# Optimization experiments

Hardware: AMD Instinct MI355X
Metric: run time of the kernel (lower is better)

## Reference

```python
import jax, jax.numpy as jnp
import numpy as np

N_HEAD, D_MODEL, D_K, D_V = 16, 1024, 64, 64
LN_EPS = 1e-5


def setup_inputs() -> dict:
    key = jax.random.key(0)
    ks = jax.random.split(key, 10)
    B, S = 2, 2048
    s = 1.0 / np.sqrt(D_MODEL)
    return {
        "q": jax.random.normal(ks[0], (B, S, D_MODEL), jnp.float32),
        "k": jax.random.normal(ks[1], (B, S, D_MODEL), jnp.float32),
        "v": jax.random.normal(ks[2], (B, S, D_MODEL), jnp.float32),
        "w_q": jax.random.normal(ks[3], (D_MODEL, N_HEAD * D_K), jnp.float32) * s,
        "w_k": jax.random.normal(ks[4], (D_MODEL, N_HEAD * D_K), jnp.float32) * s,
        "w_v": jax.random.normal(ks[5], (D_MODEL, N_HEAD * D_V), jnp.float32) * s,
        "w_fc": jax.random.normal(ks[6], (N_HEAD * D_V, D_MODEL), jnp.float32) * s,
        "b_fc": jnp.zeros((D_MODEL,), jnp.float32),
        "ln_g": jnp.ones((D_MODEL,), jnp.float32),
        "ln_b": jnp.zeros((D_MODEL,), jnp.float32),
    }


def _mha(q, k, v, w_q, w_k, w_v, w_fc, b_fc, ln_g, ln_b):
    B, S, _ = q.shape
    residual = q
    # projections -> [B, H, S, Dh]
    qh = (q @ w_q).reshape(B, S, N_HEAD, D_K).transpose(0, 2, 1, 3)
    kh = (k @ w_k).reshape(B, S, N_HEAD, D_K).transpose(0, 2, 1, 3)
    vh = (v @ w_v).reshape(B, S, N_HEAD, D_V).transpose(0, 2, 1, 3)
    # NOTE: original scales by sqrt(d_model), not sqrt(d_k)
    temper = jnp.sqrt(jnp.asarray(D_MODEL, qh.dtype))
    attn = jnp.einsum("bhqd,bhkd->bhqk", qh, kh) / temper
    attn = jax.nn.softmax(attn, axis=-1)  # dropout = identity (eval mode)
    out = jnp.einsum("bhqk,bhkd->bhqd", attn, vh)
    out = out.transpose(0, 2, 1, 3).reshape(B, S, N_HEAD * D_V)
    out = out @ w_fc + b_fc  # dropout = identity (eval mode)
    x = out + residual
    mu = jnp.mean(x, axis=-1, keepdims=True)
    var = jnp.var(x, axis=-1, keepdims=True)
    x = (x - mu) * jax.lax.rsqrt(var + LN_EPS) * ln_g + ln_b
    return x, attn


def reference(q, k, v, w_q, w_k, w_v, w_fc, b_fc, ln_g, ln_b):
    return _mha(q, k, v, w_q, w_k, w_v, w_fc, b_fc, ln_g, ln_b)
```

## Files before the change

### kernel.cpp

```cpp
#include <hip/hip_runtime.h>
#include <hip/hip_bf16.h>
#include <stdint.h>

typedef __attribute__((ext_vector_type(8))) short bf16x8;
typedef __attribute__((ext_vector_type(4))) float f32x4;

#define GLOAD16(gptr, lptr)                                              \
  __builtin_amdgcn_global_load_lds(                                      \
      (const __attribute__((address_space(1))) void*)(gptr),             \
      (__attribute__((address_space(3))) void*)(lptr), 16, 0, 0)

__device__ __forceinline__ uint32_t pack_bf16_2(float a, float b) {
  union { __hip_bfloat16 h; unsigned short u; } ca, cb;
  ca.h = __float2bfloat16(a); cb.h = __float2bfloat16(b);
  return (uint32_t)ca.u | ((uint32_t)cb.u << 16);
}

__global__ __launch_bounds__(256)
void cvt_kernel(const float* __restrict__ in0, const float* __restrict__ in1,
                const float* __restrict__ in2, __hip_bfloat16* __restrict__ out0,
                __hip_bfloat16* __restrict__ out1, __hip_bfloat16* __restrict__ out2,
                int n)
{
  const int z = blockIdx.y;
  const float* in = z == 0 ? in0 : z == 1 ? in1 : in2;
  __hip_bfloat16* out = z == 0 ? out0 : z == 1 ? out1 : out2;
  long i = ((long)blockIdx.x * 256 + threadIdx.x) * 8;
  if (i + 8 > n) return;
  float4 a = *(const float4*)(in + i);
  float4 b = *(const float4*)(in + i + 4);
  uint4 r;
  r.x = pack_bf16_2(a.x, a.y); r.y = pack_bf16_2(a.z, a.w);
  r.z = pack_bf16_2(b.x, b.y); r.w = pack_bf16_2(b.z, b.w);
  *(uint4*)(out + i) = r;
}

__global__ __launch_bounds__(256)
void wtrans_kernel(const float* __restrict__ w0, const float* __restrict__ w1,
                   const float* __restrict__ w2, const float* __restrict__ w3,
                   __hip_bfloat16* __restrict__ o0, __hip_bfloat16* __restrict__ o1,
                   __hip_bfloat16* __restrict__ o2, __hip_bfloat16* __restrict__ o3)
{
  const int z = blockIdx.z;
  const float* in = z == 0 ? w0 : z == 1 ? w1 : z == 2 ? w2 : w3;
  __hip_bfloat16* out = z == 0 ? o0 : z == 1 ? o1 : z == 2 ? o2 : o3;
  __shared__ float t[64][65];
  const int tx = threadIdx.x & 15, ty = threadIdx.x >> 4;
  const int bx = blockIdx.x, by = blockIdx.y;
  for (int i = 0; i < 4; ++i)
    for (int j = 0; j < 4; ++j)
      t[ty*4+i][tx*4+j] = in[(long)(by*64 + ty*4+i)*1024 + bx*64 + tx*4 + j];
  __syncthreads();
  for (int i = 0; i < 4; ++i)
    for (int j = 0; j < 4; ++j)
      out[(long)(bx*64 + ty*4+i)*1024 + by*64 + tx*4 + j] =
          __float2bfloat16(t[tx*4+j][ty*4+i]);
}

__global__ __launch_bounds__(256)
void vtrans_kernel(const __hip_bfloat16* __restrict__ in, __hip_bfloat16* __restrict__ out)
{
  __shared__ __hip_bfloat16 t[64][72];
  const int tx = threadIdx.x & 15, ty = threadIdx.x >> 4;
  const int sb = blockIdx.x, bh = blockIdx.y;
  const __hip_bfloat16* inp = in + (long)bh * 2048 * 64;
  __hip_bfloat16* outp = out + (long)bh * 64 * 2048;
  for (int i = 0; i < 4; ++i)
    for (int j = 0; j < 4; ++j)
      t[ty*4+i][tx*4+j] = inp[(long)(sb*64 + ty*4+i)*64 + tx*4 + j];
  __syncthreads();
  for (int i = 0; i < 4; ++i)
    for (int j = 0; j < 4; ++j)
      outp[(long)(ty*4+i)*2048 + sb*64 + tx*4 + j] = t[tx*4+j][ty*4+i];
}

template<int EPI>
__global__ __launch_bounds__(256)
void gemm_bt(const __hip_bfloat16* __restrict__ A0,
             const __hip_bfloat16* __restrict__ A1,
             const __hip_bfloat16* __restrict__ A2,
             const __hip_bfloat16* __restrict__ B0,
             const __hip_bfloat16* __restrict__ B1,
             const __hip_bfloat16* __restrict__ B2,
             void* __restrict__ out,
             const float* __restrict__ bias,
             const float* __restrict__ resid,
             int M, int N, int K)
{
  const int z = (EPI == 0) ? blockIdx.z : 0;
  const __hip_bfloat16* A  = z == 0 ? A0 : z == 1 ? A1 : A2;
  const __hip_bfloat16* Bt = z == 0 ? B0 : z == 1 ? B1 : B2;
  const float scale = (EPI == 0 && z == 0) ? 0.045084219f : 1.0f;

  __shared__ __hip_bfloat16 As[128*32];
  __shared__ __hip_bfloat16 Bs[128*32];
  const int tid = threadIdx.x;
  const int wid = tid >> 6;
  const int lane = tid & 63;
  const int lr = lane & 15, lg = lane >> 4;
  const int bm = blockIdx.y, bn = blockIdx.x;
  const int wm = wid >> 1, wn = wid & 1;

  f32x4 acc[4][4] = {};

  const int srow = tid >> 2;
  const int scol = (tid & 3) * 8;
  const __hip_bfloat16* Ag = A  + (long)(bm*128 + srow)*K + scol;
  const __hip_bfloat16* Bg = Bt + (long)(bn*128 + srow)*K + scol;
  __hip_bfloat16* AsW = &As[wid*512];
  __hip_bfloat16* BsW = &Bs[wid*512];

  for (int k0 = 0; k0 < K; k0 += 32) {
    GLOAD16(Ag + k0,          AsW);
    GLOAD16(Ag + 64*K + k0,   AsW + 2048);
    GLOAD16(Bg + k0,          BsW);
    GLOAD16(Bg + 64*K + k0,   BsW + 2048);
    __syncthreads();
    bf16x8 a[4], b[4];
    for (int m = 0; m < 4; ++m)
      a[m] = *(const bf16x8*)&As[(wm*64 + m*16 + lr)*32 + lg*8];
    for (int n = 0; n < 4; ++n)
      b[n] = *(const bf16x8*)&Bs[(wn*64 + n*16 + lr)*32 + lg*8];
    for (int m = 0; m < 4; ++m)
      for (int n = 0; n < 4; ++n)
        acc[m][n] = __builtin_amdgcn_mfma_f32_16x16x32_bf16(b[n], a[m], acc[m][n], 0, 0, 0);
    __syncthreads();
  }

  for (int m = 0; m < 4; ++m) {
    const int grow = bm*128 + wm*64 + m*16 + lr;
    for (int n = 0; n < 4; ++n) {
      const int c0 = bn*128 + wn*64 + n*16 + lg*4;
      if (EPI == 0) {
        const int b_ = grow >> 11, s = grow & 2047;
        const int h = c0 >> 6, d = c0 & 63;
        uint2 pk;
        pk.x = pack_bf16_2(acc[m][n][0]*scale, acc[m][n][1]*scale);
        pk.y = pack_bf16_2(acc[m][n][2]*scale, acc[m][n][3]*scale);
        *(uint2*)((__hip_bfloat16*)out + (long)z*4194304 +
                  ((long)(b_*16 + h)*2048 + s)*64 + d) = pk;
      } else {
        float4 b4 = *(const float4*)(bias + c0);
        float4 r4 = *(const float4*)(resid + (long)grow*N + c0);
        float4 o4;
        o4.x = acc[m][n][0] + b4.x + r4.x;
        o4.y = acc[m][n][1] + b4.y + r4.y;
        o4.z = acc[m][n][2] + b4.z + r4.z;
        o4.w = acc[m][n][3] + b4.w + r4.w;
        *(float4*)((float*)out + (long)grow*N + c0) = o4;
      }
    }
  }
}

__global__ __launch_bounds__(256)
void attn_kernel(const __hip_bfloat16* __restrict__ Qh,
                 const __hip_bfloat16* __restrict__ Kh,
                 const __hip_bfloat16* __restrict__ Vt,
                 float* __restrict__ attn_out,
                 __hip_bfloat16* __restrict__ O)
{
  __shared__ __hip_bfloat16 Ps[64*128];
  __shared__ float red[4][64];
  __shared__ float invl[64];

  const int tid = threadIdx.x, wid = tid >> 6, lane = tid & 63;
  const int lr = lane & 15, lg = lane >> 4;
  const int qb = blockIdx.x, bh = blockIdx.y;

  const __hip_bfloat16* Qlane = Qh + ((long)bh*2048 + qb*64 + lr)*64 + lg*8;
  const __hip_bfloat16* Klane = Kh + (long)bh*2048*64 + (long)(wid*32 + lr)*64 + lg*8;
  const __hip_bfloat16* Vlane = Vt + (long)bh*64*2048 + (long)(wid*16 + lr)*2048 + lg*8;

  bf16x8 aq[4][2];
  for (int mq = 0; mq < 4; ++mq)
    for (int kk = 0; kk < 2; ++kk)
      aq[mq][kk] = *(const bf16x8*)(Qlane + mq*1024 + kk*32);

  float rs[4] = {0.f, 0.f, 0.f, 0.f};
  for (int kt = 0; kt < 16; ++kt) {
    bf16x8 bk[2][2];
    for (int nk = 0; nk < 2; ++nk)
      for (int kk = 0; kk < 2; ++kk)
        bk[nk][kk] = *(const bf16x8*)(Klane + kt*8192 + nk*1024 + kk*32);
    f32x4 s2[4][2] = {};
    for (int mq = 0; mq < 4; ++mq)
      for (int nk = 0; nk < 2; ++nk)
        for (int kk = 0; kk < 2; ++kk)
          s2[mq][nk] = __builtin_amdgcn_mfma_f32_16x16x32_bf16(bk[nk][kk], aq[mq][kk], s2[mq][nk], 0, 0, 0);
    for (int mq = 0; mq < 4; ++mq)
      for (int nk = 0; nk < 2; ++nk)
        for (int jj = 0; jj < 4; ++jj)
          rs[mq] += exp2f(s2[mq][nk][jj]);
  }

  for (int mq = 0; mq < 4; ++mq) {
    float e = rs[mq];
    e += __shfl_xor(e, 16);
    e += __shfl_xor(e, 32);
    rs[mq] = e;
  }
  if (lg == 0)
    for (int mq = 0; mq < 4; ++mq)
      red[wid][mq*16 + lr] = rs[mq];
  __syncthreads();
  if (tid < 64)
    invl[tid] = 1.0f / (red[0][tid] + red[1][tid] + red[2][tid] + red[3][tid]);
  __syncthreads();

  float iv[4];
  for (int mq = 0; mq < 4; ++mq) iv[mq] = invl[mq*16 + lr];

  f32x4 acc_o[4] = {};
  float* attn_row = attn_out + ((long)bh*2048 + qb*64)*2048;

  for (int kt = 0; kt < 16; ++kt) {
    bf16x8 bk[2][2];
    for (int nk = 0; nk < 2; ++nk)
      for (int kk = 0; kk < 2; ++kk)
        bk[nk][kk] = *(const bf16x8*)(Klane + kt*8192 + nk*1024 + kk*32);
    bf16x8 vb[4];
    for (int k2 = 0; k2 < 4; ++k2)
      vb[k2] = *(const bf16x8*)(Vlane + kt*128 + k2*32);

    f32x4 s2[4][2] = {};
    for (int mq = 0; mq < 4; ++mq)
      for (int nk = 0; nk < 2; ++nk)
        for (int kk = 0; kk < 2; ++kk)
          s2[mq][nk] = __builtin_amdgcn_mfma_f32_16x16x32_bf16(bk[nk][kk], aq[mq][kk], s2[mq][nk], 0, 0, 0);

    for (int mq = 0; mq < 4; ++mq) {
      const int row = mq*16 + lr;
      for (int nk = 0; nk < 2; ++nk) {
        const int kc = wid*32 + nk*16 + lg*4;
        f32x4 p;
        p[0] = exp2f(s2[mq][nk][0]) * iv[mq];
        p[1] = exp2f(s2[mq][nk][1]) * iv[mq];
        p[2] = exp2f(s2[mq][nk][2]) * iv[mq];
        p[3] = exp2f(s2[mq][nk][3]) * iv[mq];
        __builtin_nontemporal_store(p, (f32x4*)(attn_row + (long)row*2048 + kt*128 + kc));
        uint2 pb;
        pb.x = pack_bf16_2(p[0], p[1]);
        pb.y = pack_bf16_2(p[2], p[3]);
        const int boff = (row*256 + kc*2) ^ ((row & 15) << 4);
        *(uint2*)((char*)Ps + boff) = pb;
      }
    }
    __syncthreads();

    for (int mq = 0; mq < 4; ++mq) {
      const int row = mq*16 + lr;
      for (int k2 = 0; k2 < 4; ++k2) {
        const int boff = (row*256 + (k2*32 + lg*8)*2) ^ ((row & 15) << 4);
        bf16x8 pa = *(const bf16x8*)((char*)Ps + boff);
        acc_o[mq] = __builtin_amdgcn_mfma_f32_16x16x32_bf16(vb[k2], pa, acc_o[mq], 0, 0, 0);
      }
    }
    __syncthreads();
  }

  const int b_ = bh >> 4, h = bh & 15;
  for (int mq = 0; mq < 4; ++mq) {
    const long grow = (long)b_*2048 + qb*64 + mq*16 + lr;
    const int col = h*64 + wid*16 + lg*4;
    uint2 pk;
    pk.x = pack_bf16_2(acc_o[mq][0], acc_o[mq][1]);
    pk.y = pack_bf16_2(acc_o[mq][2], acc_o[mq][3]);
    *(uint2*)(O + grow*1024 + col) = pk;
  }
}

__global__ __launch_bounds__(256)
void ln_kernel(const float* __restrict__ xin, const float* __restrict__ gam,
               const float* __restrict__ bet, float* __restrict__ xout)
{
  const int row = blockIdx.x;
  const int tid = threadIdx.x;
  const float* xr = xin + (long)row*1024;
  float4 v = *(const float4*)(xr + tid*4);
  float s  = v.x + v.y + v.z + v.w;
  float ss = v.x*v.x + v.y*v.y + v.z*v.z + v.w*v.w;
  for (int o = 1; o < 64; o <<= 1) {
    s  += __shfl_xor(s, o, 64);
    ss += __shfl_xor(ss, o, 64);
  }
  __shared__ float rsh[4], rssh[4];
  const int wid = tid >> 6, lane = tid & 63;
  if (lane == 0) { rsh[wid] = s; rssh[wid] = ss; }
  __syncthreads();
  s  = rsh[0] + rsh[1] + rsh[2] + rsh[3];
  ss = rssh[0] + rssh[1] + rssh[2] + rssh[3];
  const float mean = s * (1.0f/1024.0f);
  const float var  = ss * (1.0f/1024.0f) - mean*mean;
  const float rstd = rsqrtf(var + 1e-5f);
  float4 g4 = *(const float4*)(gam + tid*4);
  float4 b4 = *(const float4*)(bet + tid*4);
  float4 o4;
  o4.x = (v.x - mean)*rstd*g4.x + b4.x;
  o4.y = (v.y - mean)*rstd*g4.y + b4.y;
  o4.z = (v.z - mean)*rstd*g4.z + b4.z;
  o4.w = (v.w - mean)*rstd*g4.w + b4.w;
  *(float4*)(xout + (long)row*1024 + tid*4) = o4;
}

extern "C" void kernel_launch(void* const* d_in, const int* in_sizes, int n_in,
                              void* d_out, int out_size, void* d_ws, size_t ws_size,
                              hipStream_t stream)
{
  (void)in_sizes; (void)n_in; (void)out_size; (void)ws_size;
  const float* q    = (const float*)d_in[0];
  const float* k    = (const float*)d_in[1];
  const float* v    = (const float*)d_in[2];
  const float* w_q  = (const float*)d_in[3];
  const float* w_k  = (const float*)d_in[4];
  const float* w_v  = (const float*)d_in[5];
  const float* w_fc = (const float*)d_in[6];
  const float* b_fc = (const float*)d_in[7];
  const float* ln_g = (const float*)d_in[8];
  const float* ln_b = (const float*)d_in[9];

  const long MB = 1024*1024;
  char* ws = (char*)d_ws;
  __hip_bfloat16* q_bf  = (__hip_bfloat16*)(ws);
  __hip_bfloat16* k_bf  = (__hip_bfloat16*)(ws +  8*MB);
  __hip_bfloat16* v_bf  = (__hip_bfloat16*)(ws + 16*MB);
  __hip_bfloat16* wq_t  = (__hip_bfloat16*)(ws + 24*MB);
  __hip_bfloat16* wk_t  = (__hip_bfloat16*)(ws + 26*MB);
  __hip_bfloat16* wv_t  = (__hip_bfloat16*)(ws + 28*MB);
  __hip_bfloat16* wfc_t = (__hip_bfloat16*)(ws + 30*MB);
  __hip_bfloat16* QKVh  = (__hip_bfloat16*)(ws + 32*MB);
  __hip_bfloat16* Qh    = QKVh;
  __hip_bfloat16* Kh    = QKVh + 4194304L;
  __hip_bfloat16* Vh    = QKVh + 8388608L;
  __hip_bfloat16* Vht   = (__hip_bfloat16*)(ws + 56*MB);
  __hip_bfloat16* Obuf  = (__hip_bfloat16*)(ws + 64*MB);
  float*          xbuf  = (float*)(ws + 72*MB);

  float* x_out    = (float*)d_out;
  float* attn_out = x_out + 4194304L;

  const int NQ = 4096*1024;
  cvt_kernel<<<dim3(NQ/2048, 3), 256, 0, stream>>>(q, k, v, q_bf, k_bf, v_bf, NQ);

  wtrans_kernel<<<dim3(16, 16, 4), 256, 0, stream>>>(w_q, w_k, w_v, w_fc,
                                                     wq_t, wk_t, wv_t, wfc_t);

  gemm_bt<0><<<dim3(8, 32, 3), 256, 0, stream>>>(q_bf, k_bf, v_bf,
                                                 wq_t, wk_t, wv_t,
                                                 QKVh, nullptr, nullptr, 4096, 1024, 1024);

  vtrans_kernel<<<dim3(32, 32), 256, 0, stream>>>(Vh, Vht);

  attn_kernel<<<dim3(32, 32), 256, 0, stream>>>(Qh, Kh, Vht, attn_out, Obuf);

  gemm_bt<2><<<dim3(8, 32), 256, 0, stream>>>(Obuf, nullptr, nullptr,
                                              wfc_t, nullptr, nullptr,
                                              xbuf, b_fc, q, 4096, 1024, 1024);

  ln_kernel<<<4096, 256, 0, stream>>>(xbuf, ln_g, ln_b, x_out);
}
```

Measured before the change: 288.6 us.

## Prefetch next K/V tile in attention loop, remap blocks per XCD, raise MFMA priority

The attention kernel's second pass now loads the next iteration's K and V fragments into registers while the current tile's exp/store and PV MFMAs run, hiding global load latency. The grid becomes 1D with a remap so consecutive blocks on the same XCD share a batch-head, improving L2 reuse of K/V. s_setprio raises wave priority around MFMA sections. In exchange it uses more registers, which could reduce occupancy.

```diff
diff --git a/kernel.cpp b/kernel.cpp
--- a/kernel.cpp
+++ b/kernel.cpp
@@ -166,7 +166,8 @@
 
   const int tid = threadIdx.x, wid = tid >> 6, lane = tid & 63;
   const int lr = lane & 15, lg = lane >> 4;
-  const int qb = blockIdx.x, bh = blockIdx.y;
+  const int orig = (blockIdx.x & 7) * 128 + (blockIdx.x >> 3);
+  const int bh = orig >> 5, qb = orig & 31;
 
   const __hip_bfloat16* Qlane = Qh + ((long)bh*2048 + qb*64 + lr)*64 + lg*8;
   const __hip_bfloat16* Klane = Kh + (long)bh*2048*64 + (long)(wid*32 + lr)*64 + lg*8;
@@ -214,21 +215,38 @@
   f32x4 acc_o[4] = {};
   float* attn_row = attn_out + ((long)bh*2048 + qb*64)*2048;
 
+  bf16x8 bk[2][2], vb[4];
+#pragma unroll
+  for (int nk = 0; nk < 2; ++nk)
+    for (int kk = 0; kk < 2; ++kk)
+      bk[nk][kk] = *(const bf16x8*)(Klane + nk*1024 + kk*32);
+#pragma unroll
+  for (int k2 = 0; k2 < 4; ++k2)
+    vb[k2] = *(const bf16x8*)(Vlane + k2*32);
+
+#pragma unroll 1
   for (int kt = 0; kt < 16; ++kt) {
-    bf16x8 bk[2][2];
-    for (int nk = 0; nk < 2; ++nk)
-      for (int kk = 0; kk < 2; ++kk)
-        bk[nk][kk] = *(const bf16x8*)(Klane + kt*8192 + nk*1024 + kk*32);
-    bf16x8 vb[4];
-    for (int k2 = 0; k2 < 4; ++k2)
-      vb[k2] = *(const bf16x8*)(Vlane + kt*128 + k2*32);
-
     f32x4 s2[4][2] = {};
+    __builtin_amdgcn_s_setprio(1);
+#pragma unroll
     for (int mq = 0; mq < 4; ++mq)
       for (int nk = 0; nk < 2; ++nk)
         for (int kk = 0; kk < 2; ++kk)
           s2[mq][nk] = __builtin_amdgcn_mfma_f32_16x16x32_bf16(bk[nk][kk], aq[mq][kk], s2[mq][nk], 0, 0, 0);
-
+    __builtin_amdgcn_s_setprio(0);
+
+    bf16x8 nbk[2][2], nvb[4];
+    if (kt < 15) {
+#pragma unroll
+      for (int nk = 0; nk < 2; ++nk)
+        for (int kk = 0; kk < 2; ++kk)
+          nbk[nk][kk] = *(const bf16x8*)(Klane + (kt+1)*8192 + nk*1024 + kk*32);
+#pragma unroll
+      for (int k2 = 0; k2 < 4; ++k2)
+        nvb[k2] = *(const bf16x8*)(Vlane + (kt+1)*128 + k2*32);
+    }
+
+#pragma unroll
     for (int mq = 0; mq < 4; ++mq) {
       const int row = mq*16 + lr;
       for (int nk = 0; nk < 2; ++nk) {
@@ -248,6 +266,8 @@
     }
     __syncthreads();
 
+    __builtin_amdgcn_s_setprio(1);
+#pragma unroll
     for (int mq = 0; mq < 4; ++mq) {
       const int row = mq*16 + lr;
       for (int k2 = 0; k2 < 4; ++k2) {
@@ -256,7 +276,16 @@
         acc_o[mq] = __builtin_amdgcn_mfma_f32_16x16x32_bf16(vb[k2], pa, acc_o[mq], 0, 0, 0);
       }
     }
+    __builtin_amdgcn_s_setprio(0);
     __syncthreads();
+
+#pragma unroll
+    for (int nk = 0; nk < 2; ++nk)
+      for (int kk = 0; kk < 2; ++kk)
+        bk[nk][kk] = nbk[nk][kk];
+#pragma unroll
+    for (int k2 = 0; k2 < 4; ++k2)
+      vb[k2] = nvb[k2];
   }
 
   const int b_ = bh >> 4, h = bh & 15;
@@ -351,7 +380,7 @@
 
   vtrans_kernel<<<dim3(32, 32), 256, 0, stream>>>(Vh, Vht);
 
-  attn_kernel<<<dim3(32, 32), 256, 0, stream>>>(Qh, Kh, Vht, attn_out, Obuf);
+  attn_kernel<<<1024, 256, 0, stream>>>(Qh, Kh, Vht, attn_out, Obuf);
 
   gemm_bt<2><<<dim3(8, 32), 256, 0, stream>>>(Obuf, nullptr, nullptr,
                                               wfc_t, nullptr, nullptr,
```

Measured after the change: 278.5 us. 1.04x faster.
